# Performance work log

Hardware: AMD Instinct MI355X
Metric: run time of the kernel (lower is better)

Reference implementation:

```python
import jax, jax.numpy as jnp
import numpy as np

N_IMAGE, N_REGIONS = 128, 36
N_CAPTION, N_WORD = 128, 32
D = 1024
LAMBDA_SOFTMAX = 20.0
EPS = 1e-8
LEAKY_SLOPE = 0.1


def setup_inputs() -> dict:
    key = jax.random.key(0)
    k1, k2 = jax.random.split(key)
    images = jax.random.normal(k1, (N_IMAGE, N_REGIONS, D), dtype=jnp.float32)
    captions = jax.random.normal(k2, (N_CAPTION, N_WORD, D), dtype=jnp.float32)
    # all captions at max length so the per-caption loop vectorizes exactly
    cap_lens = jnp.full((N_CAPTION,), N_WORD, dtype=jnp.int32)
    return {"images": images, "captions": captions, "cap_lens": cap_lens}


def _l2norm(x, axis):
    return x / (jnp.linalg.norm(x, axis=axis, keepdims=True) + EPS)


def _focal_attn(raw):
    # raw: (..., S, Q) = context @ query^T, as in torch bmm(context, queryT)
    a = jax.nn.leaky_relu(raw, LEAKY_SLOPE)
    a = _l2norm(a, axis=-1)              # l2norm over queryL (dim=2 in torch)
    a = jnp.swapaxes(a, -1, -2)          # (..., Q, S)
    a = jax.nn.softmax(a * LAMBDA_SOFTMAX, axis=-1)
    # focal_equal: funcF = attn*S - sum_j attn_j ; mask where positive
    S = a.shape[-1]
    funcF = a * S - jnp.sum(a, axis=-1, keepdims=True)
    fattn = jnp.where(funcF > 0, 1.0, 0.0).astype(a.dtype)
    tmp = fattn * a
    return tmp / jnp.sum(tmp, axis=-1, keepdims=True)  # renormalized attn (..., Q, S)


def _cosine(a, b):
    # torch F.cosine_similarity semantics along last axis
    na = jnp.maximum(jnp.linalg.norm(a, axis=-1), EPS)
    nb = jnp.maximum(jnp.linalg.norm(b, axis=-1), EPS)
    return jnp.sum(a * b, axis=-1) / (na * nb)


def reference(images, captions, cap_lens):
    # images: (I, R, d); captions: (C, W, d); all cap_lens == W (vectorized loop)
    # ---- t2i: query = caption words, context = image regions ----
    raw_t2i = jnp.einsum('ird,cwd->cirw', images, captions)   # (C, I, R=S, W=Q)
    re_t2i = _focal_attn(raw_t2i)                             # (C, I, W, R)
    wctx_t2i = jnp.einsum('ciwr,ird->ciwd', re_t2i, images)   # (C, I, W, d)
    t2i = _cosine(captions[:, None, :, :], wctx_t2i).mean(axis=-1)  # (C, I)
    # ---- i2t: query = image regions, context = caption words ----
    raw_i2t = jnp.einsum('cwd,ird->ciwr', captions, images)   # (C, I, W=S, R=Q)
    re_i2t = _focal_attn(raw_i2t)                             # (C, I, R, W)
    wctx_i2t = jnp.einsum('cirw,cwd->cird', re_i2t, captions) # (C, I, R, d)
    i2t = _cosine(images[None, :, :, :], wctx_i2t).mean(axis=-1)    # (C, I)
    return (t2i + i2t).T                                      # (n_image, n_caption)
```

## Files before the change

kernel.cpp:

```cpp
#include <hip/hip_runtime.h>
#include <math.h>

#define NR 36
#define NW 32
#define DD 1024
#define EPSF 1e-8f

typedef _Float16 f16x8 __attribute__((ext_vector_type(8)));
typedef float f32x16 __attribute__((ext_vector_type(16)));
#define MFMA32(a, b, c) __builtin_amdgcn_mfma_f32_32x32x16_f16((a), (b), (c), 0, 0, 0)
#define GLD16(srcp, dstp)                                                              \
  __builtin_amdgcn_global_load_lds((const __attribute__((address_space(1))) void*)(srcp), \
                                   (__attribute__((address_space(3))) void*)(dstp), 16, 0, 0)

__device__ __forceinline__ float leakyf(float x) { return x > 0.f ? x : 0.1f * x; }

__global__ __launch_bounds__(256) void prep_kernel(
    const float* __restrict__ img, const float* __restrict__ cap,
    float* __restrict__ Gimg, float* __restrict__ Gcap,
    float* __restrict__ imgn, float* __restrict__ capn,
    _Float16* __restrict__ Ahf, _Float16* __restrict__ Alf,
    _Float16* __restrict__ Bhf, _Float16* __restrict__ Blf) {
  __shared__ float sA[2][NR][64];
  const int t = threadIdx.x;
  if (blockIdx.x < 128) {
    const int i = blockIdx.x;
    const float* A = img + (size_t)i * NR * DD;
    int ti = 0, tj = 0;
    const bool active = t < 171;
    if (active) {
      int rem = t, rl = 18;
      while (rem >= rl) { rem -= rl; ++ti; --rl; }
      tj = ti + rem;
    }
    const int a0 = 2 * ti, a1 = 2 * ti + 1, b0 = 2 * tj, b1 = 2 * tj + 1;
    const int sza = ti & 7, szb = tj & 7;
    const int kq8_1 = t / NR, r1 = t - kq8_1 * NR;
    const bool has2 = t < 32;
    const int s2 = t + 256;
    const int kq8_2 = s2 / NR, r2 = s2 - kq8_2 * NR;
    float4 p0a, p1a, p0b, p1b;
    float g00 = 0.f, g01 = 0.f, g10 = 0.f, g11 = 0.f;

    auto loadRegs = [&](int idx) {
      const int k0 = idx * 64;
      p0a = *(const float4*)(A + r1 * DD + k0 + kq8_1 * 8);
      p1a = *(const float4*)(A + r1 * DD + k0 + kq8_1 * 8 + 4);
      if (has2) {
        p0b = *(const float4*)(A + r2 * DD + k0 + kq8_2 * 8);
        p1b = *(const float4*)(A + r2 * DD + k0 + kq8_2 * 8 + 4);
      }
    };
    auto cw = [&](int idx, int cur) {
      const int k0 = idx * 64;
      {
        const float a[8] = {p0a.x, p0a.y, p0a.z, p0a.w, p1a.x, p1a.y, p1a.z, p1a.w};
        f16x8 hv;
#pragma unroll
        for (int j = 0; j < 8; ++j) hv[j] = (_Float16)a[j];
        const int m = i * NR + r1, mt = m >> 5, ml = m & 31;
        const int kk = k0 + kq8_1 * 8;
        const size_t fo = (((size_t)mt * 128 + (kk >> 3)) * 32 + ml) * 8;
        *(f16x8*)(Ahf + fo) = hv;
        const int sw = (r1 >> 1) & 7;
        *(float4*)&sA[cur][r1][((2 * kq8_1) ^ sw) * 4] = p0a;
        *(float4*)&sA[cur][r1][((2 * kq8_1 + 1) ^ sw) * 4] = p1a;
      }
      if (has2) {
        const float a[8] = {p0b.x, p0b.y, p0b.z, p0b.w, p1b.x, p1b.y, p1b.z, p1b.w};
        f16x8 hv;
#pragma unroll
        for (int j = 0; j < 8; ++j) hv[j] = (_Float16)a[j];
        const int m = i * NR + r2, mt = m >> 5, ml = m & 31;
        const int kk = k0 + kq8_2 * 8;
        const size_t fo = (((size_t)mt * 128 + (kk >> 3)) * 32 + ml) * 8;
        *(f16x8*)(Ahf + fo) = hv;
        const int sw = (r2 >> 1) & 7;
        *(float4*)&sA[cur][r2][((2 * kq8_2) ^ sw) * 4] = p0b;
        *(float4*)&sA[cur][r2][((2 * kq8_2 + 1) ^ sw) * 4] = p1b;
      }
    };

    loadRegs(0);
    for (int idx = 0; idx < 16; ++idx) {
      const int cur = idx & 1;
      cw(idx, cur);
      if (idx < 15) loadRegs(idx + 1);
      __syncthreads();
      if (active) {
#pragma unroll
        for (int k = 0; k < 16; ++k) {
          const float4 va0 = *(const float4*)&sA[cur][a0][(k ^ sza) * 4];
          const float4 va1 = *(const float4*)&sA[cur][a1][(k ^ sza) * 4];
          const float4 vb0 = *(const float4*)&sA[cur][b0][(k ^ szb) * 4];
          const float4 vb1 = *(const float4*)&sA[cur][b1][(k ^ szb) * 4];
          g00 = fmaf(va0.x, vb0.x, g00); g00 = fmaf(va0.y, vb0.y, g00);
          g00 = fmaf(va0.z, vb0.z, g00); g00 = fmaf(va0.w, vb0.w, g00);
          g01 = fmaf(va0.x, vb1.x, g01); g01 = fmaf(va0.y, vb1.y, g01);
          g01 = fmaf(va0.z, vb1.z, g01); g01 = fmaf(va0.w, vb1.w, g01);
          g10 = fmaf(va1.x, vb0.x, g10); g10 = fmaf(va1.y, vb0.y, g10);
          g10 = fmaf(va1.z, vb0.z, g10); g10 = fmaf(va1.w, vb0.w, g10);
          g11 = fmaf(va1.x, vb1.x, g11); g11 = fmaf(va1.y, vb1.y, g11);
          g11 = fmaf(va1.z, vb1.z, g11); g11 = fmaf(va1.w, vb1.w, g11);
        }
      }
    }
    if (active) {
      float* Gi = Gimg + (size_t)i * NR * NR;
      Gi[a0 * NR + b0] = g00; Gi[b0 * NR + a0] = g00;
      Gi[a0 * NR + b1] = g01; Gi[b1 * NR + a0] = g01;
      Gi[a1 * NR + b0] = g10; Gi[b0 * NR + a1] = g10;
      Gi[a1 * NR + b1] = g11; Gi[b1 * NR + a1] = g11;
      if (ti == tj) {
        imgn[i * NR + a0] = fmaxf(sqrtf(g00), EPSF);
        imgn[i * NR + a1] = fmaxf(sqrtf(g11), EPSF);
      }
    }
  } else {
    const int cb = blockIdx.x - 128;
    const float* A = cap + (size_t)cb * NW * DD;
    int ti = 0, tj = 0;
    const bool active = t < 136;
    if (active) {
      int rem = t, rl = 16;
      while (rem >= rl) { rem -= rl; ++ti; --rl; }
      tj = ti + rem;
    }
    const int a0 = 2 * ti, a1 = 2 * ti + 1, b0 = 2 * tj, b1 = 2 * tj + 1;
    const int sza = ti & 7, szb = tj & 7;
    const int kq8_1 = t >> 5, r1 = t & 31;
    float4 p0a, p1a;
    float g00 = 0.f, g01 = 0.f, g10 = 0.f, g11 = 0.f;

    auto loadRegs = [&](int idx) {
      const int k0 = idx * 64;
      p0a = *(const float4*)(A + r1 * DD + k0 + kq8_1 * 8);
      p1a = *(const float4*)(A + r1 * DD + k0 + kq8_1 * 8 + 4);
    };
    auto cw = [&](int idx, int cur) {
      const int k0 = idx * 64;
      const float a[8] = {p0a.x, p0a.y, p0a.z, p0a.w, p1a.x, p1a.y, p1a.z, p1a.w};
      f16x8 hv;
#pragma unroll
      for (int j = 0; j < 8; ++j) hv[j] = (_Float16)a[j];
      const int kk = k0 + kq8_1 * 8;
      const size_t fo = (((size_t)cb * 128 + (kk >> 3)) * 32 + r1) * 8;
      *(f16x8*)(Bhf + fo) = hv;
      const int sw = (r1 >> 1) & 7;
      *(float4*)&sA[cur][r1][((2 * kq8_1) ^ sw) * 4] = p0a;
      *(float4*)&sA[cur][r1][((2 * kq8_1 + 1) ^ sw) * 4] = p1a;
    };

    loadRegs(0);
    for (int idx = 0; idx < 16; ++idx) {
      const int cur = idx & 1;
      cw(idx, cur);
      if (idx < 15) loadRegs(idx + 1);
      __syncthreads();
      if (active) {
#pragma unroll
        for (int k = 0; k < 16; ++k) {
          const float4 va0 = *(const float4*)&sA[cur][a0][(k ^ sza) * 4];
          const float4 va1 = *(const float4*)&sA[cur][a1][(k ^ sza) * 4];
          const float4 vb0 = *(const float4*)&sA[cur][b0][(k ^ szb) * 4];
          const float4 vb1 = *(const float4*)&sA[cur][b1][(k ^ szb) * 4];
          g00 = fmaf(va0.x, vb0.x, g00); g00 = fmaf(va0.y, vb0.y, g00);
          g00 = fmaf(va0.z, vb0.z, g00); g00 = fmaf(va0.w, vb0.w, g00);
          g01 = fmaf(va0.x, vb1.x, g01); g01 = fmaf(va0.y, vb1.y, g01);
          g01 = fmaf(va0.z, vb1.z, g01); g01 = fmaf(va0.w, vb1.w, g01);
          g10 = fmaf(va1.x, vb0.x, g10); g10 = fmaf(va1.y, vb0.y, g10);
          g10 = fmaf(va1.z, vb0.z, g10); g10 = fmaf(va1.w, vb0.w, g10);
          g11 = fmaf(va1.x, vb1.x, g11); g11 = fmaf(va1.y, vb1.y, g11);
          g11 = fmaf(va1.z, vb1.z, g11); g11 = fmaf(va1.w, vb1.w, g11);
        }
      }
    }
    if (active) {
      float* Gc = Gcap + (size_t)cb * NW * NW;
      Gc[a0 * NW + b0] = g00; Gc[b0 * NW + a0] = g00;
      Gc[a0 * NW + b1] = g01; Gc[b1 * NW + a0] = g01;
      Gc[a1 * NW + b0] = g10; Gc[b0 * NW + a1] = g10;
      Gc[a1 * NW + b1] = g11; Gc[b1 * NW + a1] = g11;
      if (ti == tj) {
        capn[cb * NW + a0] = fmaxf(sqrtf(g00), EPSF);
        capn[cb * NW + a1] = fmaxf(sqrtf(g11), EPSF);
      }
    }
  }
}

__device__ __forceinline__ void gemm_loadA(const _Float16* __restrict__ Ahf, int Mt0, int kt,
                                           int kb, int lm, f16x8 ar[2][2]) {
#pragma unroll
  for (int mt = 0; mt < 2; ++mt)
#pragma unroll
    for (int ks = 0; ks < 2; ++ks) {
      const size_t o = (((size_t)(Mt0 + mt) * 128) + kt * 4 + ks * 2 + kb) * 256 + lm * 8;
      ar[mt][ks] = *(const f16x8*)(Ahf + o);
    }
}

__global__ __launch_bounds__(256) void mfma_gemm_kernel(
    const _Float16* __restrict__ Ahf, const _Float16* __restrict__ Alf,
    const _Float16* __restrict__ Bhf, const _Float16* __restrict__ Blf, float* __restrict__ C) {
  __shared__ _Float16 sB[2][4096];
  const int bid0 = blockIdx.x;
  const int bid = (bid0 & 7) * 144 + (bid0 >> 3);
  const int yb = bid & 31, xb = bid >> 5;
  const int n0b = yb * 4;
  const int tid = threadIdx.x;
  const int wv = tid >> 6, lane = tid & 63;
  const int lm = lane & 31, kb = lane >> 5;
  const int Mt0 = xb * 4 + (wv >> 1) * 2;
  const int nb0 = (wv & 1) * 2;
  (void)Alf; (void)Blf;

  auto stageB = [&](int kt, int buf) {
#pragma unroll
    for (int u = 0; u < 2; ++u) {
      const int cpb = wv * 4 + u * 2;
      const int cp = cpb + kb;
      const int nb = cp >> 2, kq = cp & 3;
      const _Float16* src = Bhf + (((size_t)(n0b + nb) * 128 + kt * 4 + kq) * 32 + lm) * 8;
      GLD16(src, &sB[buf][cpb * 256]);
    }
  };

  f32x16 acc[2][2];
#pragma unroll
  for (int a = 0; a < 2; ++a)
#pragma unroll
    for (int b = 0; b < 2; ++b) acc[a][b] = {};
  f16x8 ar0[2][2], ar1[2][2];

  auto computeBuf = [&](const _Float16* sb, const f16x8 ar[2][2]) {
#pragma unroll
    for (int ks = 0; ks < 2; ++ks)
#pragma unroll
      for (int ntl = 0; ntl < 2; ++ntl) {
        const int nt = nb0 + ntl;
        const int co = (nt * 4 + ks * 2 + kb) * 256 + lm * 8;
        const f16x8 bh = *(const f16x8*)&sb[co];
        acc[0][ntl] = MFMA32(ar[0][ks], bh, acc[0][ntl]);
        acc[1][ntl] = MFMA32(ar[1][ks], bh, acc[1][ntl]);
      }
  };

  stageB(0, 0);
  gemm_loadA(Ahf, Mt0, 0, kb, lm, ar0);
  for (int kt2 = 0; kt2 < 16; ++kt2) {
    const int kt = kt2 * 2;
    __syncthreads();
    if (kt + 1 < 32) {
      stageB(kt + 1, 1);
      gemm_loadA(Ahf, Mt0, kt + 1, kb, lm, ar1);
    }
    computeBuf(sB[0], ar0);
    __syncthreads();
    if (kt + 2 < 32) {
      stageB(kt + 2, 0);
      gemm_loadA(Ahf, Mt0, kt + 2, kb, lm, ar0);
    }
    computeBuf(sB[1], ar1);
  }
#pragma unroll
  for (int mt = 0; mt < 2; ++mt)
#pragma unroll
    for (int ntl = 0; ntl < 2; ++ntl) {
      const int cc = n0b + nb0 + ntl;
      const f32x16 a = acc[mt][ntl];
#pragma unroll
      for (int q = 0; q < 16; ++q) {
        const int row32 = (q & 3) + 8 * (q >> 2) + 4 * kb;
        const int m = (Mt0 + mt) * 32 + row32;
        const int il = m / NR, r = m - il * NR;
        C[((size_t)il * 128 + cc) * (NR * NW) + r * NW + lm] = a[q];
      }
    }
}

__global__ __launch_bounds__(512, 4) void fused_attn_kernel(
    const float* __restrict__ C, const float* __restrict__ Gimg, const float* __restrict__ Gcap,
    const float* __restrict__ imgn, const float* __restrict__ capn, float* __restrict__ out) {
  const int i = blockIdx.x;
  const int cg = blockIdx.y;
  const int tid = threadIdx.x;
  const int wv = tid >> 6, lane = tid & 63;
  __shared__ float sS[8][NR * 36];
  __shared__ float sInvR[8][NR];
  __shared__ float sInvC[8][NW];
  __shared__ float red[8];
  if (tid < 8) red[tid] = 0.f;
  const float* Cp = C + ((size_t)i * 128 + cg * 8) * (NR * NW);
  for (int t = tid; t < 8 * NR * NW / 4; t += 512) {
    const int cap = t / (NR * NW / 4);
    const int rem = t - cap * (NR * NW / 4);
    const int r = rem >> 3, wq = rem & 7;
    const float4 v = *(const float4*)(Cp + cap * (NR * NW) + r * NW + wq * 4);
    *(float4*)&sS[cap][r * 36 + wq * 4] = v;
  }
  __syncthreads();
  if (tid < 256) {
    const int capT = tid >> 5, wT = tid & 31;
    float cn = 0.f;
#pragma unroll
    for (int j = 0; j < NR; ++j) {
      const float l = leakyf(sS[capT][j * 36 + wT]);
      cn = fmaf(l, l, cn);
    }
    sInvC[capT][wT] = 20.f / (sqrtf(cn) + EPSF);
  } else {
    const int u = tid - 256;
    {
      const int cap = u >> 5, r = u & 31;
      float rn = 0.f;
#pragma unroll
      for (int k = 0; k < 8; ++k) {
        const float4 v = *(const float4*)&sS[cap][r * 36 + k * 4];
        float l;
        l = leakyf(v.x); rn = fmaf(l, l, rn);
        l = leakyf(v.y); rn = fmaf(l, l, rn);
        l = leakyf(v.z); rn = fmaf(l, l, rn);
        l = leakyf(v.w); rn = fmaf(l, l, rn);
      }
      sInvR[cap][r] = 20.f / (sqrtf(rn) + EPSF);
    }
    if (u < 32) {
      const int cap = u >> 2, r = 32 + (u & 3);
      float rn = 0.f;
#pragma unroll
      for (int k = 0; k < 8; ++k) {
        const float4 v = *(const float4*)&sS[cap][r * 36 + k * 4];
        float l;
        l = leakyf(v.x); rn = fmaf(l, l, rn);
        l = leakyf(v.y); rn = fmaf(l, l, rn);
        l = leakyf(v.z); rn = fmaf(l, l, rn);
        l = leakyf(v.w); rn = fmaf(l, l, rn);
      }
      sInvR[cap][r] = 20.f / (sqrtf(rn) + EPSF);
    }
  }
  __syncthreads();
  if (tid < 256) {
    const int capT = tid >> 5, wT = tid & 31;
    float s[NR], z[NR];
#pragma unroll
    for (int j = 0; j < NR; ++j) s[j] = sS[capT][j * 36 + wT];
    float mz = -1e30f;
#pragma unroll
    for (int j = 0; j < NR; ++j) {
      z[j] = leakyf(s[j]) * sInvR[capT][j];
      mz = fmaxf(mz, z[j]);
    }
    float s1 = 0.f;
#pragma unroll
    for (int j = 0; j < NR; ++j) { z[j] = __expf(z[j] - mz); s1 += z[j]; }
    const float thr = s1 * (1.f / NR);
    float num = 0.f;
#pragma unroll
    for (int j = 0; j < NR; ++j) {
      z[j] = (z[j] > thr) ? z[j] : 0.f;
      num = fmaf(z[j], s[j], num);
    }
    const float* Gp = Gimg + (size_t)i * (NR * NR);
    float den2 = 0.f;
#pragma unroll
    for (int j = 0; j < NR; ++j) {
      float h = 0.5f * z[j] * Gp[j * NR + j];
#pragma unroll
      for (int j2 = j + 1; j2 < NR; ++j2) h = fmaf(z[j2], Gp[j * NR + j2], h);
      den2 = fmaf(z[j], h, den2);
    }
    const float val = num / (capn[(cg * 8 + capT) * NW + wT] * sqrtf(2.f * den2) + 1e-30f);
    float contrib = val * (1.f / NW);
#pragma unroll
    for (int d = 1; d < 32; d <<= 1) contrib += __shfl_xor(contrib, d, 64);
    if ((tid & 31) == 0) atomicAdd(&red[capT], contrib);
  } else {
    const int wv2 = wv - 4;
#pragma unroll
    for (int it = 0; it < 2; ++it) {
      const int capu = wv2 + it * 4;
      const int cglob = cg * 8 + capu;
      float contrib = 0.f;
      if (lane < NR) {
        float sr[NW], z[NW];
#pragma unroll
        for (int k = 0; k < 8; ++k)
          *(float4*)&sr[k * 4] = *(const float4*)&sS[capu][lane * 36 + k * 4];
        float mz = -1e30f;
#pragma unroll
        for (int w = 0; w < NW; ++w) {
          z[w] = leakyf(sr[w]) * sInvC[capu][w];
          mz = fmaxf(mz, z[w]);
        }
        float s1 = 0.f;
#pragma unroll
        for (int w = 0; w < NW; ++w) { z[w] = __expf(z[w] - mz); s1 += z[w]; }
        const float thr = s1 * (1.f / NW);
        float num = 0.f;
#pragma unroll
        for (int w = 0; w < NW; ++w) {
          z[w] = (z[w] > thr) ? z[w] : 0.f;
          num = fmaf(z[w], sr[w], num);
        }
        const float* Gp = Gcap + (size_t)cglob * (NW * NW);
        float den2 = 0.f;
#pragma unroll
        for (int w = 0; w < NW; ++w) {
          float h = 0.5f * z[w] * Gp[w * NW + w];
#pragma unroll
          for (int w2 = w + 1; w2 < NW; ++w2) h = fmaf(z[w2], Gp[w * NW + w2], h);
          den2 = fmaf(z[w], h, den2);
        }
        const float val = num / (imgn[i * NR + lane] * sqrtf(2.f * den2) + 1e-30f);
        contrib = val * (1.f / NR);
      }
#pragma unroll
      for (int d = 1; d < 64; d <<= 1) contrib += __shfl_xor(contrib, d, 64);
      if (lane == 0) atomicAdd(&red[capu], contrib);
    }
  }
  __syncthreads();
  if (tid < 8) out[(size_t)i * 128 + cg * 8 + tid] = red[tid];
}

extern "C" void kernel_launch(void* const* d_in, const int* in_sizes, int n_in,
                              void* d_out, int out_size, void* d_ws, size_t ws_size,
                              hipStream_t stream) {
  (void)in_sizes; (void)n_in; (void)out_size; (void)ws_size;
  const float* images = (const float*)d_in[0];
  const float* captions = (const float*)d_in[1];
  float* out = (float*)d_out;

  char* wb = (char*)d_ws;
  _Float16* Ahf = (_Float16*)wb; wb += (size_t)4608 * 1024 * 2;
  _Float16* Alf = (_Float16*)wb; wb += (size_t)4608 * 1024 * 2;
  _Float16* Bhf = (_Float16*)wb; wb += (size_t)4096 * 1024 * 2;
  _Float16* Blf = (_Float16*)wb; wb += (size_t)4096 * 1024 * 2;
  float* Gimg = (float*)wb; wb += (size_t)128 * NR * NR * 4;
  float* Gcap = (float*)wb; wb += (size_t)128 * NW * NW * 4;
  float* imgn = (float*)wb; wb += (size_t)128 * NR * 4;
  float* capn = (float*)wb; wb += (size_t)128 * NW * 4;
  float* C = (float*)wb;

  prep_kernel<<<256, 256, 0, stream>>>(images, captions, Gimg, Gcap, imgn, capn,
                                       Ahf, Alf, Bhf, Blf);
  mfma_gemm_kernel<<<1152, 256, 0, stream>>>(Ahf, Alf, Bhf, Blf, C);
  fused_attn_kernel<<<dim3(128, 16), 512, 0, stream>>>(C, Gimg, Gcap, imgn, capn, out);
}
```

Measured before the change: 259.5 us.

## Stage Gram matrices in LDS and split attention blocks to 4 captions

The fused attention kernel now copies the image and caption Gram matrices into shared memory and computes the quadratic form with full-row float4 dot products, replacing scalar upper-triangle reads from global memory. Each block now handles 4 captions instead of 8, with 384 threads: one i2t wave per caption instead of two-iteration loops, and the grid doubles to 4096 blocks. The aim is to remove repeated global loads of G and the serial inner loop, at the cost of more LDS traffic, twice the FMAs in the full (non-triangular) quadratic form, and more block overhead.

```diff
diff --git a/kernel.cpp b/kernel.cpp
--- a/kernel.cpp
+++ b/kernel.cpp
@@ -279,77 +279,69 @@
     }
 }
 
-__global__ __launch_bounds__(512, 4) void fused_attn_kernel(
+__global__ __launch_bounds__(384) void fused_attn_kernel(
     const float* __restrict__ C, const float* __restrict__ Gimg, const float* __restrict__ Gcap,
     const float* __restrict__ imgn, const float* __restrict__ capn, float* __restrict__ out) {
   const int i = blockIdx.x;
   const int cg = blockIdx.y;
   const int tid = threadIdx.x;
   const int wv = tid >> 6, lane = tid & 63;
-  __shared__ float sS[8][NR * 36];
-  __shared__ float sInvR[8][NR];
-  __shared__ float sInvC[8][NW];
-  __shared__ float red[8];
-  if (tid < 8) red[tid] = 0.f;
-  const float* Cp = C + ((size_t)i * 128 + cg * 8) * (NR * NW);
-  for (int t = tid; t < 8 * NR * NW / 4; t += 512) {
-    const int cap = t / (NR * NW / 4);
-    const int rem = t - cap * (NR * NW / 4);
+  __shared__ float sS[4][NR * 36];
+  __shared__ float sGi[NR * NR];
+  __shared__ float sGc[4][NW * NW];
+  __shared__ float sInvR[4][NR];
+  __shared__ float sInvC[4][NW];
+  __shared__ float red[4];
+  if (tid < 4) red[tid] = 0.f;
+  const float* Cp = C + ((size_t)i * 128 + cg * 4) * (NR * NW);
+  for (int t = tid; t < 4 * 288; t += 384) {
+    const int cap = t / 288, rem = t - cap * 288;
     const int r = rem >> 3, wq = rem & 7;
     const float4 v = *(const float4*)(Cp + cap * (NR * NW) + r * NW + wq * 4);
     *(float4*)&sS[cap][r * 36 + wq * 4] = v;
   }
+  const float* Gi = Gimg + (size_t)i * (NR * NR);
+  for (int t = tid; t < 324; t += 384) *(float4*)&sGi[t * 4] = *(const float4*)(Gi + t * 4);
+  const float* Gc0 = Gcap + (size_t)(cg * 4) * (NW * NW);
+  for (int t = tid; t < 1024; t += 384) {
+    const int cap = t >> 8, q = t & 255;
+    *(float4*)&sGc[cap][q * 4] = *(const float4*)(Gc0 + cap * (NW * NW) + q * 4);
+  }
   __syncthreads();
-  if (tid < 256) {
-    const int capT = tid >> 5, wT = tid & 31;
+  if (tid < 128) {
+    const int cap = tid >> 5, w = tid & 31;
     float cn = 0.f;
 #pragma unroll
     for (int j = 0; j < NR; ++j) {
-      const float l = leakyf(sS[capT][j * 36 + wT]);
+      const float l = leakyf(sS[cap][j * 36 + w]);
       cn = fmaf(l, l, cn);
     }
-    sInvC[capT][wT] = 20.f / (sqrtf(cn) + EPSF);
-  } else {
-    const int u = tid - 256;
-    {
-      const int cap = u >> 5, r = u & 31;
-      float rn = 0.f;
-#pragma unroll
-      for (int k = 0; k < 8; ++k) {
-        const float4 v = *(const float4*)&sS[cap][r * 36 + k * 4];
-        float l;
-        l = leakyf(v.x); rn = fmaf(l, l, rn);
-        l = leakyf(v.y); rn = fmaf(l, l, rn);
-        l = leakyf(v.z); rn = fmaf(l, l, rn);
-        l = leakyf(v.w); rn = fmaf(l, l, rn);
-      }
-      sInvR[cap][r] = 20.f / (sqrtf(rn) + EPSF);
-    }
-    if (u < 32) {
-      const int cap = u >> 2, r = 32 + (u & 3);
-      float rn = 0.f;
-#pragma unroll
-      for (int k = 0; k < 8; ++k) {
-        const float4 v = *(const float4*)&sS[cap][r * 36 + k * 4];
-        float l;
-        l = leakyf(v.x); rn = fmaf(l, l, rn);
-        l = leakyf(v.y); rn = fmaf(l, l, rn);
-        l = leakyf(v.z); rn = fmaf(l, l, rn);
-        l = leakyf(v.w); rn = fmaf(l, l, rn);
-      }
-      sInvR[cap][r] = 20.f / (sqrtf(rn) + EPSF);
-    }
+    sInvC[cap][w] = 20.f / (sqrtf(cn) + EPSF);
+  } else if (tid < 272) {
+    const int u = tid - 128;
+    const int cap = u / NR, r = u - cap * NR;
+    float rn = 0.f;
+#pragma unroll
+    for (int k = 0; k < 8; ++k) {
+      const float4 v = *(const float4*)&sS[cap][r * 36 + k * 4];
+      float l;
+      l = leakyf(v.x); rn = fmaf(l, l, rn);
+      l = leakyf(v.y); rn = fmaf(l, l, rn);
+      l = leakyf(v.z); rn = fmaf(l, l, rn);
+      l = leakyf(v.w); rn = fmaf(l, l, rn);
+    }
+    sInvR[cap][r] = 20.f / (sqrtf(rn) + EPSF);
   }
   __syncthreads();
-  if (tid < 256) {
-    const int capT = tid >> 5, wT = tid & 31;
+  if (tid < 128) {
+    const int cap = tid >> 5, w = tid & 31;
     float s[NR], z[NR];
 #pragma unroll
-    for (int j = 0; j < NR; ++j) s[j] = sS[capT][j * 36 + wT];
+    for (int j = 0; j < NR; ++j) s[j] = sS[cap][j * 36 + w];
     float mz = -1e30f;
 #pragma unroll
     for (int j = 0; j < NR; ++j) {
-      z[j] = leakyf(s[j]) * sInvR[capT][j];
+      z[j] = leakyf(s[j]) * sInvR[cap][j];
       mz = fmaxf(mz, z[j]);
     }
     float s1 = 0.f;
@@ -362,67 +354,72 @@
       z[j] = (z[j] > thr) ? z[j] : 0.f;
       num = fmaf(z[j], s[j], num);
     }
-    const float* Gp = Gimg + (size_t)i * (NR * NR);
     float den2 = 0.f;
 #pragma unroll
     for (int j = 0; j < NR; ++j) {
-      float h = 0.5f * z[j] * Gp[j * NR + j];
-#pragma unroll
-      for (int j2 = j + 1; j2 < NR; ++j2) h = fmaf(z[j2], Gp[j * NR + j2], h);
+      float h = 0.f;
+#pragma unroll
+      for (int k = 0; k < 9; ++k) {
+        const float4 g = *(const float4*)&sGi[j * 36 + k * 4];
+        h = fmaf(g.x, z[k * 4 + 0], h);
+        h = fmaf(g.y, z[k * 4 + 1], h);
+        h = fmaf(g.z, z[k * 4 + 2], h);
+        h = fmaf(g.w, z[k * 4 + 3], h);
+      }
       den2 = fmaf(z[j], h, den2);
     }
-    const float val = num / (capn[(cg * 8 + capT) * NW + wT] * sqrtf(2.f * den2) + 1e-30f);
+    const float val = num / (capn[(cg * 4 + cap) * NW + w] * sqrtf(den2) + 1e-30f);
     float contrib = val * (1.f / NW);
 #pragma unroll
     for (int d = 1; d < 32; d <<= 1) contrib += __shfl_xor(contrib, d, 64);
-    if ((tid & 31) == 0) atomicAdd(&red[capT], contrib);
-  } else {
-    const int wv2 = wv - 4;
-#pragma unroll
-    for (int it = 0; it < 2; ++it) {
-      const int capu = wv2 + it * 4;
-      const int cglob = cg * 8 + capu;
-      float contrib = 0.f;
-      if (lane < NR) {
-        float sr[NW], z[NW];
-#pragma unroll
-        for (int k = 0; k < 8; ++k)
-          *(float4*)&sr[k * 4] = *(const float4*)&sS[capu][lane * 36 + k * 4];
-        float mz = -1e30f;
-#pragma unroll
-        for (int w = 0; w < NW; ++w) {
-          z[w] = leakyf(sr[w]) * sInvC[capu][w];
-          mz = fmaxf(mz, z[w]);
+    if ((tid & 31) == 0) atomicAdd(&red[cap], contrib);
+  } else if (wv >= 2) {
+    const int capu = wv - 2;
+    float contrib = 0.f;
+    if (lane < NR) {
+      float sr[NW], z[NW];
+#pragma unroll
+      for (int k = 0; k < 8; ++k)
+        *(float4*)&sr[k * 4] = *(const float4*)&sS[capu][lane * 36 + k * 4];
+      float mz = -1e30f;
+#pragma unroll
+      for (int w = 0; w < NW; ++w) {
+        z[w] = leakyf(sr[w]) * sInvC[capu][w];
+        mz = fmaxf(mz, z[w]);
+      }
+      float s1 = 0.f;
+#pragma unroll
+      for (int w = 0; w < NW; ++w) { z[w] = __expf(z[w] - mz); s1 += z[w]; }
+      const float thr = s1 * (1.f / NW);
+      float num = 0.f;
+#pragma unroll
+      for (int w = 0; w < NW; ++w) {
+        z[w] = (z[w] > thr) ? z[w] : 0.f;
+        num = fmaf(z[w], sr[w], num);
+      }
+      float den2 = 0.f;
+#pragma unroll
+      for (int w = 0; w < NW; ++w) {
+        float h = 0.f;
+#pragma unroll
+        for (int k = 0; k < 8; ++k) {
+          const float4 g = *(const float4*)&sGc[capu][w * 32 + k * 4];
+          h = fmaf(g.x, z[k * 4 + 0], h);
+          h = fmaf(g.y, z[k * 4 + 1], h);
+          h = fmaf(g.z, z[k * 4 + 2], h);
+          h = fmaf(g.w, z[k * 4 + 3], h);
         }
-        float s1 = 0.f;
-#pragma unroll
-        for (int w = 0; w < NW; ++w) { z[w] = __expf(z[w] - mz); s1 += z[w]; }
-        const float thr = s1 * (1.f / NW);
-        float num = 0.f;
-#pragma unroll
-        for (int w = 0; w < NW; ++w) {
-          z[w] = (z[w] > thr) ? z[w] : 0.f;
-          num = fmaf(z[w], sr[w], num);
-        }
-        const float* Gp = Gcap + (size_t)cglob * (NW * NW);
-        float den2 = 0.f;
-#pragma unroll
-        for (int w = 0; w < NW; ++w) {
-          float h = 0.5f * z[w] * Gp[w * NW + w];
-#pragma unroll
-          for (int w2 = w + 1; w2 < NW; ++w2) h = fmaf(z[w2], Gp[w * NW + w2], h);
-          den2 = fmaf(z[w], h, den2);
-        }
-        const float val = num / (imgn[i * NR + lane] * sqrtf(2.f * den2) + 1e-30f);
-        contrib = val * (1.f / NR);
-      }
-#pragma unroll
-      for (int d = 1; d < 64; d <<= 1) contrib += __shfl_xor(contrib, d, 64);
-      if (lane == 0) atomicAdd(&red[capu], contrib);
-    }
+        den2 = fmaf(z[w], h, den2);
+      }
+      const float val = num / (imgn[i * NR + lane] * sqrtf(den2) + 1e-30f);
+      contrib = val * (1.f / NR);
+    }
+#pragma unroll
+    for (int d = 1; d < 64; d <<= 1) contrib += __shfl_xor(contrib, d, 64);
+    if (lane == 0) atomicAdd(&red[capu], contrib);
   }
   __syncthreads();
-  if (tid < 8) out[(size_t)i * 128 + cg * 8 + tid] = red[tid];
+  if (tid < 4) out[(size_t)i * 128 + cg * 4 + tid] = red[tid];
 }
 
 extern "C" void kernel_launch(void* const* d_in, const int* in_sizes, int n_in,
@@ -447,5 +444,5 @@
   prep_kernel<<<256, 256, 0, stream>>>(images, captions, Gimg, Gcap, imgn, capn,
                                        Ahf, Alf, Bhf, Blf);
   mfma_gemm_kernel<<<1152, 256, 0, stream>>>(Ahf, Alf, Bhf, Blf, C);
-  fused_attn_kernel<<<dim3(128, 16), 512, 0, stream>>>(C, Gimg, Gcap, imgn, capn, out);
+  fused_attn_kernel<<<dim3(128, 32), 384, 0, stream>>>(C, Gimg, Gcap, imgn, capn, out);
 }
```

After: 261.3 us. About the same (+0.7%).
